# Optimization experiments

Hardware: AMD Instinct MI355X
Metric: run time of the kernel (lower is better)

## Reference

```python
import jax, jax.numpy as jnp
import numpy as np

B, T, C, D = 4, 4096, 1024, 64

def setup_inputs() -> dict:
    key = jax.random.key(0)
    k1, k2, k3, k4 = jax.random.split(key, 4)
    return {
        "x": jax.random.normal(k1, (B, T, C), dtype=jnp.float32),
        "Wq": jax.random.normal(k2, (C, D), dtype=jnp.float32) * (C ** -0.5),
        "Wk": jax.random.normal(k3, (C, D), dtype=jnp.float32) * (C ** -0.5),
        "Wv": jax.random.normal(k4, (C, D), dtype=jnp.float32) * (C ** -0.5),
    }

def reference(x, Wq, Wk, Wv):
    # Single-head causal self-attention (context defaults to x; dropout p=0 -> identity)
    T_ = x.shape[1]
    Q = jnp.einsum('btc,cd->btd', x, Wq)
    K = jnp.einsum('btc,cd->btd', x, Wk)
    V = jnp.einsum('btc,cd->btd', x, Wv)
    scores = jnp.einsum('btd,bsd->bts', Q, K) / jnp.sqrt(jnp.float32(K.shape[-1]))
    causal = jnp.tril(jnp.ones((T_, T_), dtype=bool))  # [T, T]
    scores = jnp.where(causal, scores, -jnp.inf)
    attn = jax.nn.softmax(scores, axis=-1)
    out = jnp.einsum('bts,bsd->btd', attn, V)
    return out
```

## Files before the change

kernel.cpp:

```cpp
#include <hip/hip_runtime.h>

typedef short bf16x8 __attribute__((ext_vector_type(8)));
typedef float f32x4 __attribute__((ext_vector_type(4)));
typedef float f32x16 __attribute__((ext_vector_type(16)));
typedef unsigned short u16;
typedef unsigned int u32;

#define MFMA_BF16 __builtin_amdgcn_mfma_f32_16x16x32_bf16
#define MFMA32 __builtin_amdgcn_mfma_f32_32x32x16_bf16

static __device__ __forceinline__ u16 f2bf(float f) {
  union { float f; unsigned u; } v; v.f = f;
  return (u16)((v.u + 0x7FFFu + ((v.u >> 16) & 1u)) >> 16);
}
static __device__ __forceinline__ u32 cvtpk(float lo, float hi) {
  u32 r;
  asm("v_cvt_pk_bf16_f32 %0, %1, %2" : "=v"(r) : "v"(lo), "v"(hi));
  return r;
}
static __device__ __forceinline__ bf16x8 cvt8(uint4 p, uint4 q) {
  union { u32 w[4]; bf16x8 b; } r;
  r.w[0] = cvtpk(__uint_as_float(p.x), __uint_as_float(p.y));
  r.w[1] = cvtpk(__uint_as_float(p.z), __uint_as_float(p.w));
  r.w[2] = cvtpk(__uint_as_float(q.x), __uint_as_float(q.y));
  r.w[3] = cvtpk(__uint_as_float(q.z), __uint_as_float(q.w));
  return r.b;
}
static __device__ __forceinline__ float xhalf(float x) { return __shfl_xor(x, 32); }
static __device__ __forceinline__ u32 xhalfu(u32 x) { return (u32)__shfl_xor((int)x, 32); }

static __device__ __forceinline__ void gload16(const void* g, void* l) {
  __builtin_amdgcn_global_load_lds(
      (const __attribute__((address_space(1))) u32*)g,
      (__attribute__((address_space(3))) u32*)l, 16, 0, 0);
}

__global__ __launch_bounds__(256) void wt_kernel(const float* __restrict__ Wq,
                                                 const float* __restrict__ Wk,
                                                 const float* __restrict__ Wv,
                                                 u16* __restrict__ Wt) {
  const int nrow = blockIdx.x;
  const int m = nrow >> 6, n = nrow & 63;
  const float* W = (m == 0) ? Wq : ((m == 1) ? Wk : Wv);
  const float s = (m == 0) ? 0.125f * 1.44269504f : 1.0f;
  for (int k = threadIdx.x; k < 1024; k += 256)
    Wt[(size_t)nrow * 1024 + k] = f2bf(W[(size_t)k * 64 + n] * s);
}

__global__ __launch_bounds__(256) void qkv6(const float* __restrict__ x,
                                            const u16* __restrict__ Wt,
                                            u16* __restrict__ Qb,
                                            u16* __restrict__ Kb,
                                            u16* __restrict__ Vt) {
  __shared__ __align__(16) char sh[2][32 * 1024];
  const int w = threadIdx.x >> 6, l = threadIdx.x & 63;
  const int lane16 = l & 15, laneHi = l >> 4;
  const int r0 = blockIdx.x * 32;
  const int nt0 = w * 3;

  const f32x4 fzero = {0.f, 0.f, 0.f, 0.f};
  f32x4 acc0 = fzero, acc1 = fzero, acc2 = fzero;
  f32x4 acc3 = fzero, acc4 = fzero, acc5 = fzero;

  auto stage = [&](int buf, int s) {
    char* base = &sh[buf][0];
    const int k0 = s * 64;
    if (w < 3) {
#pragma unroll
      for (int ii = 0; ii < 8; ++ii) {
        const int nt = w * 4 + (ii >> 1), kh = ii & 1;
        const u16* g = Wt + (size_t)(nt * 16 + lane16) * 1024 + k0 + kh * 32 + laneHi * 8;
        gload16(g, base + (nt * 2 + kh) * 1024);
      }
    } else {
#pragma unroll
      for (int ii = 0; ii < 8; ++ii) {
        const int m = ii >> 2, kh = (ii >> 1) & 1, p = ii & 1;
        const float* g = x + (size_t)(r0 + m * 16 + lane16) * 1024 + k0 + kh * 32 + laneHi * 8 + p * 4;
        gload16(g, base + (24 + ii) * 1024);
      }
    }
  };

  auto comp = [&](int buf) {
    const char* base = &sh[buf][0] + (size_t)l * 16;
    bf16x8 b00 = *(const bf16x8*)(base + ((nt0 + 0) * 2 + 0) * 1024);
    bf16x8 b01 = *(const bf16x8*)(base + ((nt0 + 0) * 2 + 1) * 1024);
    bf16x8 b10 = *(const bf16x8*)(base + ((nt0 + 1) * 2 + 0) * 1024);
    bf16x8 b11 = *(const bf16x8*)(base + ((nt0 + 1) * 2 + 1) * 1024);
    bf16x8 b20 = *(const bf16x8*)(base + ((nt0 + 2) * 2 + 0) * 1024);
    bf16x8 b21 = *(const bf16x8*)(base + ((nt0 + 2) * 2 + 1) * 1024);
    uint4 x00a = *(const uint4*)(base + 24 * 1024);
    uint4 x00b = *(const uint4*)(base + 25 * 1024);
    uint4 x01a = *(const uint4*)(base + 26 * 1024);
    uint4 x01b = *(const uint4*)(base + 27 * 1024);
    uint4 x10a = *(const uint4*)(base + 28 * 1024);
    uint4 x10b = *(const uint4*)(base + 29 * 1024);
    uint4 x11a = *(const uint4*)(base + 30 * 1024);
    uint4 x11b = *(const uint4*)(base + 31 * 1024);
    bf16x8 a00 = cvt8(x00a, x00b);
    bf16x8 a01 = cvt8(x01a, x01b);
    bf16x8 a10 = cvt8(x10a, x10b);
    bf16x8 a11 = cvt8(x11a, x11b);
    acc0 = MFMA_BF16(a00, b00, acc0, 0, 0, 0);
    acc0 = MFMA_BF16(a01, b01, acc0, 0, 0, 0);
    acc1 = MFMA_BF16(a00, b10, acc1, 0, 0, 0);
    acc1 = MFMA_BF16(a01, b11, acc1, 0, 0, 0);
    acc2 = MFMA_BF16(a00, b20, acc2, 0, 0, 0);
    acc2 = MFMA_BF16(a01, b21, acc2, 0, 0, 0);
    acc3 = MFMA_BF16(a10, b00, acc3, 0, 0, 0);
    acc3 = MFMA_BF16(a11, b01, acc3, 0, 0, 0);
    acc4 = MFMA_BF16(a10, b10, acc4, 0, 0, 0);
    acc4 = MFMA_BF16(a11, b11, acc4, 0, 0, 0);
    acc5 = MFMA_BF16(a10, b20, acc5, 0, 0, 0);
    acc5 = MFMA_BF16(a11, b21, acc5, 0, 0, 0);
  };

  stage(0, 0);
  __syncthreads();
#pragma unroll 1
  for (int s = 0; s < 16; ++s) {
    if (s + 1 < 16) stage((s + 1) & 1, s + 1);
    comp(s & 1);
    __syncthreads();
  }

#define ST(AC, m, i)                                                        \
  {                                                                         \
    const int nt = nt0 + (i);                                               \
    if (nt < 4) {                                                           \
      _Pragma("unroll")                                                     \
      for (int r = 0; r < 4; ++r)                                           \
        Qb[(size_t)(r0 + (m) * 16 + laneHi * 4 + r) * 64 + nt * 16 + lane16] = f2bf(AC[r]); \
    } else if (nt < 8) {                                                    \
      _Pragma("unroll")                                                     \
      for (int r = 0; r < 4; ++r)                                           \
        Kb[(size_t)(r0 + (m) * 16 + laneHi * 4 + r) * 64 + (nt - 4) * 16 + lane16] = f2bf(AC[r]); \
    } else {                                                                \
      const int d = (nt - 8) * 16 + lane16;                                 \
      uint2 v;                                                              \
      v.x = cvtpk(AC[0], AC[1]);                                            \
      v.y = cvtpk(AC[2], AC[3]);                                            \
      *(uint2*)(Vt + (size_t)d * 16384 + r0 + (m) * 16 + laneHi * 4) = v;   \
    }                                                                       \
  }

  ST(acc0, 0, 0) ST(acc1, 0, 1) ST(acc2, 0, 2)
  ST(acc3, 1, 0) ST(acc4, 1, 1) ST(acc5, 1, 2)
}

__global__ __launch_bounds__(512) void attn6(const u16* __restrict__ Qb,
                                             const u16* __restrict__ Kb,
                                             const u16* __restrict__ Vt,
                                             float* __restrict__ out) {
  __shared__ float shC[4][64][37];
  __shared__ __align__(16) float shT[32][68];

  const int tid = threadIdx.x, w = tid >> 6, l = tid & 63;
  const int q = l & 31, hi = l >> 5;
  const bool isHi = hi != 0;
  const int b = blockIdx.x & 3;
  const int j = blockIdx.x >> 2;
  const int t = (j >> 6) ? (j & 63) : (127 - (j & 63));
  const int q0 = t * 32, bT = b * 4096;

  const u16* qp = Qb + (size_t)(bT + q0 + q) * 64 + 8 * hi;
  const bf16x8 qf0 = *(const bf16x8*)(qp);
  const bf16x8 qf1 = *(const bf16x8*)(qp + 16);
  const bf16x8 qf2 = *(const bf16x8*)(qp + 32);
  const bf16x8 qf3 = *(const bf16x8*)(qp + 48);

  const int nu = t + 1;
  const int s = (nu * w) >> 3, e = (nu * (w + 1)) >> 3;

  f32x16 o0 = {}, o1 = {};
  float m = -INFINITY, lsum = 0.f;

  bf16x8 kA[4], vA[4], kB[4], vB[4];

  auto loadKV = [&](bf16x8 (&kf)[4], bf16x8 (&vf)[4], int u) {
    const int k0 = bT + u * 32;
    const u16* kp = Kb + (size_t)(k0 + q) * 64 + 8 * hi;
#pragma unroll
    for (int kc = 0; kc < 4; ++kc) kf[kc] = *(const bf16x8*)(kp + kc * 16);
#pragma unroll
    for (int dt = 0; dt < 2; ++dt)
#pragma unroll
      for (int c = 0; c < 2; ++c)
        vf[dt * 2 + c] = *(const bf16x8*)(Vt + (size_t)(dt * 32 + q) * 16384 + k0 + c * 16 + 8 * hi);
  };

  auto compute = [&](bf16x8 (&kf)[4], bf16x8 (&vf)[4], int u) {
    f32x16 sc = {};
    __builtin_amdgcn_s_setprio(1);
    sc = MFMA32(kf[0], qf0, sc, 0, 0, 0);
    sc = MFMA32(kf[1], qf1, sc, 0, 0, 0);
    sc = MFMA32(kf[2], qf2, sc, 0, 0, 0);
    sc = MFMA32(kf[3], qf3, sc, 0, 0, 0);
    __builtin_amdgcn_s_setprio(0);

    if (u == t) {
#pragma unroll
      for (int r = 0; r < 16; ++r) {
        const int key = (r & 3) + 8 * (r >> 2) + 4 * hi;
        if (key > q) sc[r] = -INFINITY;
      }
    }

    float pm = sc[0];
#pragma unroll
    for (int r = 1; r < 16; ++r) pm = fmaxf(pm, sc[r]);
    pm = fmaxf(pm, xhalf(pm));

    if (!__all(pm <= m + 8.f)) {
      const float mn = fmaxf(m, pm);
      const float al = exp2f(fmaxf(m - mn, -80.f));
#pragma unroll
      for (int r = 0; r < 16; ++r) { o0[r] *= al; o1[r] *= al; }
      lsum *= al;
      m = mn;
    }

    float p[16];
    float rs = 0.f;
#pragma unroll
    for (int r = 0; r < 16; ++r) { p[r] = exp2f(sc[r] - m); rs += p[r]; }
    rs += xhalf(rs);
    lsum += rs;

    u32 wl0 = cvtpk(p[0], p[1]),  wl1 = cvtpk(p[2], p[3]);
    u32 wh0 = cvtpk(p[4], p[5]),  wh1 = cvtpk(p[6], p[7]);
    u32 yl0 = cvtpk(p[8], p[9]),  yl1 = cvtpk(p[10], p[11]);
    u32 yh0 = cvtpk(p[12], p[13]), yh1 = cvtpk(p[14], p[15]);
    u32 sl0 = xhalfu(wl0), sl1 = xhalfu(wl1);
    u32 sh0 = xhalfu(wh0), sh1 = xhalfu(wh1);
    u32 tl0 = xhalfu(yl0), tl1 = xhalfu(yl1);
    u32 th0 = xhalfu(yh0), th1 = xhalfu(yh1);
    union { u32 w4[4]; bf16x8 v; } pf0, pf1;
    pf0.w4[0] = isHi ? sh0 : wl0;
    pf0.w4[1] = isHi ? sh1 : wl1;
    pf0.w4[2] = isHi ? wh0 : sl0;
    pf0.w4[3] = isHi ? wh1 : sl1;
    pf1.w4[0] = isHi ? th0 : yl0;
    pf1.w4[1] = isHi ? th1 : yl1;
    pf1.w4[2] = isHi ? yh0 : tl0;
    pf1.w4[3] = isHi ? yh1 : tl1;

    __builtin_amdgcn_s_setprio(1);
    o0 = MFMA32(vf[0], pf0.v, o0, 0, 0, 0);
    o0 = MFMA32(vf[1], pf1.v, o0, 0, 0, 0);
    o1 = MFMA32(vf[2], pf0.v, o1, 0, 0, 0);
    o1 = MFMA32(vf[3], pf1.v, o1, 0, 0, 0);
    __builtin_amdgcn_s_setprio(0);
  };

  int u = s;
  if (u < e) loadKV(kA, vA, u);
#pragma unroll 1
  while (u < e) {
    if (u + 1 < e) loadKV(kB, vB, u + 1);
    compute(kA, vA, u);
    ++u;
    if (u >= e) break;
    if (u + 1 < e) loadKV(kA, vA, u + 1);
    compute(kB, vB, u);
    ++u;
  }

  auto publish = [&](int slot) {
    float* dst = &shC[slot][l][0];
    dst[0] = m; dst[1] = lsum;
#pragma unroll
    for (int r = 0; r < 16; ++r) { dst[2 + r] = o0[r]; dst[18 + r] = o1[r]; }
  };
  auto merge = [&](int slot) {
    const float* src = &shC[slot][l][0];
    const float pm = src[0], pl = src[1];
    const float mn = fmaxf(m, pm);
    const float aS = exp2f(fmaxf(m - mn, -80.f));
    const float aP = exp2f(fmaxf(pm - mn, -80.f));
    m = mn;
    lsum = lsum * aS + pl * aP;
#pragma unroll
    for (int r = 0; r < 16; ++r) {
      o0[r] = o0[r] * aS + src[2 + r] * aP;
      o1[r] = o1[r] * aS + src[18 + r] * aP;
    }
  };

  if (w >= 4) publish(w - 4);
  __syncthreads();
  if (w < 4) merge(w);
  __syncthreads();
  if (w >= 1 && w < 4) publish(w - 1);
  __syncthreads();
  if (w == 0) {
    merge(0); merge(1); merge(2);
    const float inv = 1.0f / lsum;
#pragma unroll
    for (int r = 0; r < 16; ++r) {
      const int d = (r & 3) + 8 * (r >> 2) + 4 * hi;
      shT[q][d] = o0[r] * inv;
      shT[q][32 + d] = o1[r] * inv;
    }
    __asm volatile("s_waitcnt lgkmcnt(0)" ::: "memory");
#pragma unroll
    for (int it = 0; it < 8; ++it) {
      const int row = it * 4 + (l >> 4);
      const int c4 = (l & 15) * 4;
      float4 v = *(const float4*)&shT[row][c4];
      *(float4*)(out + (size_t)(bT + q0 + row) * 64 + c4) = v;
    }
  }
}

extern "C" void kernel_launch(void* const* d_in, const int* in_sizes, int n_in,
                              void* d_out, int out_size, void* d_ws, size_t ws_size,
                              hipStream_t stream) {
  const float* x  = (const float*)d_in[0];
  const float* Wq = (const float*)d_in[1];
  const float* Wk = (const float*)d_in[2];
  const float* Wv = (const float*)d_in[3];
  float* out = (float*)d_out;

  char* ws = (char*)d_ws;
  u16* Wt = (u16*)ws;
  u16* Qb = (u16*)(ws + 393216);
  u16* Kb = (u16*)(ws + 393216 + 2097152);
  u16* Vt = (u16*)(ws + 393216 + 2 * 2097152);

  wt_kernel<<<192, 256, 0, stream>>>(Wq, Wk, Wv, Wt);
  qkv6<<<512, 256, 0, stream>>>(x, Wt, Qb, Kb, Vt);
  attn6<<<512, 512, 0, stream>>>(Qb, Kb, Vt, out);
}
```

Measured before the change: 89.88 us.

## Pair two query tiles per block to share K/V loads, retile V layout

Each attention block now handles two query tiles (tA and tA+64) at once. Every K/V tile loaded from memory is reused for both query tiles, with the tA step skipped past its diagonal, which halves the grid to 256 blocks. The V transpose written by the QKV kernel is reorganized into contiguous 32-key chunks so each V fragment load reads a compact block. The cost is more registers for the second query tile and accumulators, which may hurt occupancy, and a serialized two-pass cross-wave merge.

```diff
diff --git a/kernel.cpp b/kernel.cpp
--- a/kernel.cpp
+++ b/kernel.cpp
@@ -141,7 +141,7 @@
       uint2 v;                                                              \
       v.x = cvtpk(AC[0], AC[1]);                                            \
       v.y = cvtpk(AC[2], AC[3]);                                            \
-      *(uint2*)(Vt + (size_t)d * 16384 + r0 + (m) * 16 + laneHi * 4) = v;   \
+      *(uint2*)(Vt + ((size_t)(r0 >> 5) * 64 + d) * 32 + (m) * 16 + laneHi * 4) = v; \
     }                                                                       \
   }
 
@@ -149,10 +149,10 @@
   ST(acc3, 1, 0) ST(acc4, 1, 1) ST(acc5, 1, 2)
 }
 
-__global__ __launch_bounds__(512) void attn6(const u16* __restrict__ Qb,
-                                             const u16* __restrict__ Kb,
-                                             const u16* __restrict__ Vt,
-                                             float* __restrict__ out) {
+__global__ __launch_bounds__(512) void attn12(const u16* __restrict__ Qb,
+                                              const u16* __restrict__ Kb,
+                                              const u16* __restrict__ Vt,
+                                              float* __restrict__ out) {
   __shared__ float shC[4][64][37];
   __shared__ __align__(16) float shT[32][68];
 
@@ -160,21 +160,27 @@
   const int q = l & 31, hi = l >> 5;
   const bool isHi = hi != 0;
   const int b = blockIdx.x & 3;
-  const int j = blockIdx.x >> 2;
-  const int t = (j >> 6) ? (j & 63) : (127 - (j & 63));
-  const int q0 = t * 32, bT = b * 4096;
-
-  const u16* qp = Qb + (size_t)(bT + q0 + q) * 64 + 8 * hi;
-  const bf16x8 qf0 = *(const bf16x8*)(qp);
-  const bf16x8 qf1 = *(const bf16x8*)(qp + 16);
-  const bf16x8 qf2 = *(const bf16x8*)(qp + 32);
-  const bf16x8 qf3 = *(const bf16x8*)(qp + 48);
-
-  const int nu = t + 1;
-  const int s = (nu * w) >> 3, e = (nu * (w + 1)) >> 3;
-
-  f32x16 o0 = {}, o1 = {};
-  float m = -INFINITY, lsum = 0.f;
+  const int p_ = blockIdx.x >> 2;
+  const int tA = (p_ < 32) ? p_ : (95 - p_);
+  const int tB = tA + 64;
+  const int q0A = tA * 32, q0B = tB * 32, bT = b * 4096;
+
+  const u16* qpA = Qb + (size_t)(bT + q0A + q) * 64 + 8 * hi;
+  const bf16x8 qA0 = *(const bf16x8*)(qpA);
+  const bf16x8 qA1 = *(const bf16x8*)(qpA + 16);
+  const bf16x8 qA2 = *(const bf16x8*)(qpA + 32);
+  const bf16x8 qA3 = *(const bf16x8*)(qpA + 48);
+  const u16* qpB = Qb + (size_t)(bT + q0B + q) * 64 + 8 * hi;
+  const bf16x8 qB0 = *(const bf16x8*)(qpB);
+  const bf16x8 qB1 = *(const bf16x8*)(qpB + 16);
+  const bf16x8 qB2 = *(const bf16x8*)(qpB + 32);
+  const bf16x8 qB3 = *(const bf16x8*)(qpB + 48);
+
+  const int n = tB + 1;
+  const int s = (n * w) >> 3, e = (n * (w + 1)) >> 3;
+
+  f32x16 oA0 = {}, oA1 = {}, oB0 = {}, oB1 = {};
+  float mA = -INFINITY, lA = 0.f, mB = -INFINITY, lB = 0.f;
 
   bf16x8 kA[4], vA[4], kB[4], vB[4];
 
@@ -183,14 +189,17 @@
     const u16* kp = Kb + (size_t)(k0 + q) * 64 + 8 * hi;
 #pragma unroll
     for (int kc = 0; kc < 4; ++kc) kf[kc] = *(const bf16x8*)(kp + kc * 16);
+    const u16* vbase = Vt + (size_t)(b * 128 + u) * 2048;
 #pragma unroll
     for (int dt = 0; dt < 2; ++dt)
 #pragma unroll
       for (int c = 0; c < 2; ++c)
-        vf[dt * 2 + c] = *(const bf16x8*)(Vt + (size_t)(dt * 32 + q) * 16384 + k0 + c * 16 + 8 * hi);
-  };
-
-  auto compute = [&](bf16x8 (&kf)[4], bf16x8 (&vf)[4], int u) {
+        vf[dt * 2 + c] = *(const bf16x8*)(vbase + (dt * 32 + q) * 32 + c * 16 + 8 * hi);
+  };
+
+  auto step = [&](bf16x8 (&kf)[4], bf16x8 (&vf)[4], int u, int tdiag,
+                  const bf16x8& qf0, const bf16x8& qf1, const bf16x8& qf2, const bf16x8& qf3,
+                  float& m, float& lsum, f32x16& o0, f32x16& o1) {
     f32x16 sc = {};
     __builtin_amdgcn_s_setprio(1);
     sc = MFMA32(kf[0], qf0, sc, 0, 0, 0);
@@ -199,7 +208,7 @@
     sc = MFMA32(kf[3], qf3, sc, 0, 0, 0);
     __builtin_amdgcn_s_setprio(0);
 
-    if (u == t) {
+    if (u == tdiag) {
 #pragma unroll
       for (int r = 0; r < 16; ++r) {
         const int key = (r & 3) + 8 * (r >> 2) + 4 * hi;
@@ -254,63 +263,76 @@
     __builtin_amdgcn_s_setprio(0);
   };
 
+  auto computeU = [&](bf16x8 (&kf)[4], bf16x8 (&vf)[4], int u) {
+    if (u <= tA) step(kf, vf, u, tA, qA0, qA1, qA2, qA3, mA, lA, oA0, oA1);
+    step(kf, vf, u, tB, qB0, qB1, qB2, qB3, mB, lB, oB0, oB1);
+  };
+
   int u = s;
   if (u < e) loadKV(kA, vA, u);
 #pragma unroll 1
   while (u < e) {
     if (u + 1 < e) loadKV(kB, vB, u + 1);
-    compute(kA, vA, u);
+    computeU(kA, vA, u);
     ++u;
     if (u >= e) break;
     if (u + 1 < e) loadKV(kA, vA, u + 1);
-    compute(kB, vB, u);
+    computeU(kB, vB, u);
     ++u;
   }
 
-  auto publish = [&](int slot) {
-    float* dst = &shC[slot][l][0];
-    dst[0] = m; dst[1] = lsum;
-#pragma unroll
-    for (int r = 0; r < 16; ++r) { dst[2 + r] = o0[r]; dst[18 + r] = o1[r]; }
-  };
-  auto merge = [&](int slot) {
-    const float* src = &shC[slot][l][0];
-    const float pm = src[0], pl = src[1];
-    const float mn = fmaxf(m, pm);
-    const float aS = exp2f(fmaxf(m - mn, -80.f));
-    const float aP = exp2f(fmaxf(pm - mn, -80.f));
-    m = mn;
-    lsum = lsum * aS + pl * aP;
-#pragma unroll
-    for (int r = 0; r < 16; ++r) {
-      o0[r] = o0[r] * aS + src[2 + r] * aP;
-      o1[r] = o1[r] * aS + src[18 + r] * aP;
+#pragma unroll 1
+  for (int pass = 0; pass < 2; ++pass) {
+    float m = pass ? mB : mA, lsum = pass ? lB : lA;
+    f32x16 o0 = pass ? oB0 : oA0, o1 = pass ? oB1 : oA1;
+    const int q0 = pass ? q0B : q0A;
+
+    auto publish = [&](int slot) {
+      float* dst = &shC[slot][l][0];
+      dst[0] = m; dst[1] = lsum;
+#pragma unroll
+      for (int r = 0; r < 16; ++r) { dst[2 + r] = o0[r]; dst[18 + r] = o1[r]; }
+    };
+    auto merge = [&](int slot) {
+      const float* src = &shC[slot][l][0];
+      const float pm = src[0], pl = src[1];
+      const float mn = fmaxf(m, pm);
+      const float aS = exp2f(fmaxf(m - mn, -80.f));
+      const float aP = exp2f(fmaxf(pm - mn, -80.f));
+      m = mn;
+      lsum = lsum * aS + pl * aP;
+#pragma unroll
+      for (int r = 0; r < 16; ++r) {
+        o0[r] = o0[r] * aS + src[2 + r] * aP;
+        o1[r] = o1[r] * aS + src[18 + r] * aP;
+      }
+    };
+
+    if (w >= 4) publish(w - 4);
+    __syncthreads();
+    if (w < 4) merge(w);
+    __syncthreads();
+    if (w >= 1 && w < 4) publish(w - 1);
+    __syncthreads();
+    if (w == 0) {
+      merge(0); merge(1); merge(2);
+      const float inv = 1.0f / lsum;
+#pragma unroll
+      for (int r = 0; r < 16; ++r) {
+        const int d = (r & 3) + 8 * (r >> 2) + 4 * hi;
+        shT[q][d] = o0[r] * inv;
+        shT[q][32 + d] = o1[r] * inv;
+      }
+      __asm volatile("s_waitcnt lgkmcnt(0)" ::: "memory");
+#pragma unroll
+      for (int it = 0; it < 8; ++it) {
+        const int row = it * 4 + (l >> 4);
+        const int c4 = (l & 15) * 4;
+        float4 v = *(const float4*)&shT[row][c4];
+        *(float4*)(out + (size_t)(bT + q0 + row) * 64 + c4) = v;
+      }
     }
-  };
-
-  if (w >= 4) publish(w - 4);
-  __syncthreads();
-  if (w < 4) merge(w);
-  __syncthreads();
-  if (w >= 1 && w < 4) publish(w - 1);
-  __syncthreads();
-  if (w == 0) {
-    merge(0); merge(1); merge(2);
-    const float inv = 1.0f / lsum;
-#pragma unroll
-    for (int r = 0; r < 16; ++r) {
-      const int d = (r & 3) + 8 * (r >> 2) + 4 * hi;
-      shT[q][d] = o0[r] * inv;
-      shT[q][32 + d] = o1[r] * inv;
-    }
-    __asm volatile("s_waitcnt lgkmcnt(0)" ::: "memory");
-#pragma unroll
-    for (int it = 0; it < 8; ++it) {
-      const int row = it * 4 + (l >> 4);
-      const int c4 = (l & 15) * 4;
-      float4 v = *(const float4*)&shT[row][c4];
-      *(float4*)(out + (size_t)(bT + q0 + row) * 64 + c4) = v;
-    }
+    __syncthreads();
   }
 }
 
@@ -331,5 +353,5 @@
 
   wt_kernel<<<192, 256, 0, stream>>>(Wq, Wk, Wv, Wt);
   qkv6<<<512, 256, 0, stream>>>(x, Wt, Qb, Kb, Vt);
-  attn6<<<512, 512, 0, stream>>>(Qb, Kb, Vt, out);
-}
+  attn12<<<256, 512, 0, stream>>>(Qb, Kb, Vt, out);
+}
```

After: 88.49 us. Within noise of the previous version (-1.5%).
